# Performance work log

Hardware: AMD Instinct MI355X
Metric: run time of the kernel (lower is better)

## Reference

```python
import jax, jax.numpy as jnp
import numpy as np

B, N, D, NH, DFF = 16, 512, 1024, 16, 4096
DK = D // NH


def _layer_norm(x, eps=1e-5):
    mu = jnp.mean(x, axis=-1, keepdims=True)
    var = jnp.var(x, axis=-1, keepdims=True)
    return (x - mu) * jax.lax.rsqrt(var + eps)


def setup_inputs() -> dict:
    key = jax.random.key(0)
    ks = jax.random.split(key, 12)
    s = 0.02
    return {
        "H": jax.random.normal(ks[0], (B, N, D), jnp.float32),
        "shortest_path_matrix": jax.random.normal(ks[1], (B, N, N), jnp.float32),
        "Wq": s * jax.random.normal(ks[2], (NH, D, DK), jnp.float32),
        "bq": jnp.zeros((NH, DK), jnp.float32),
        "Wk": s * jax.random.normal(ks[3], (NH, D, DK), jnp.float32),
        "bk": jnp.zeros((NH, DK), jnp.float32),
        "Wv": s * jax.random.normal(ks[4], (NH, D, DK), jnp.float32),
        "bv": jnp.zeros((NH, DK), jnp.float32),
        "Wo": s * jax.random.normal(ks[5], (D, D), jnp.float32),
        "bo": jnp.zeros((D,), jnp.float32),
        "W1": s * jax.random.normal(ks[6], (D, DFF), jnp.float32),
        "b1": jnp.zeros((DFF,), jnp.float32),
        "W2": s * jax.random.normal(ks[7], (DFF, D), jnp.float32),
        "b2": jnp.zeros((D,), jnp.float32),
    }


def reference(H, shortest_path_matrix, Wq, bq, Wk, bk, Wv, bv, Wo, bo, W1, b1, W2, b2):
    ln1 = _layer_norm(H)  # [B,N,D]
    # per-head projections: [B,H,N,DK]
    Q = jnp.einsum('bnd,hdk->bhnk', ln1, Wq) + bq[None, :, None, :]
    K = jnp.einsum('bnd,hdk->bhnk', ln1, Wk) + bk[None, :, None, :]
    V = jnp.einsum('bnd,hdk->bhnk', ln1, Wv) + bv[None, :, None, :]
    scale = 1.0 / jnp.sqrt(jnp.asarray(DK, Q.dtype))
    scores = jnp.einsum('bhnk,bhmk->bhnm', Q, K) * scale + shortest_path_matrix[:, None, :, :]
    A = jax.nn.softmax(scores, axis=-1)
    O = jnp.einsum('bhnm,bhmk->bhnk', A, V)  # [B,H,N,DK]
    O = jnp.transpose(O, (0, 2, 1, 3)).reshape(O.shape[0], O.shape[2], -1)  # [B,N,D]
    attn_out = O @ Wo + bo
    x = attn_out + H
    h = jax.nn.relu(_layer_norm(x) @ W1 + b1)
    return x + h @ W2 + b2
```

## Files before the change

kernel.cpp:

```cpp
#include <hip/hip_runtime.h>

#define BB   16
#define NN   512
#define DD   1024
#define NHH  16
#define DKK  64
#define DFF  4096
#define MM   (BB*NN)

typedef _Float16 h16;
typedef h16  h16x8 __attribute__((ext_vector_type(8)));
typedef h16  h16x4 __attribute__((ext_vector_type(4)));
typedef float f32x4 __attribute__((ext_vector_type(4)));

#define AS1 __attribute__((address_space(1)))
#define AS3 __attribute__((address_space(3)))

__device__ __forceinline__ void gld16(h16* lds_dst, const h16* g_src) {
  __builtin_amdgcn_global_load_lds((const AS1 void*)g_src, (AS3 void*)lds_dst, 16, 0, 0);
}

__global__ __launch_bounds__(256) void ln_k(const float* __restrict__ in, h16* __restrict__ out)
{
  const int row = blockIdx.x;
  const int tid = threadIdx.x;
  const float4 v = ((const float4*)(in + (long)row * DD))[tid];
  float s  = v.x + v.y + v.z + v.w;
  float ss = v.x*v.x + v.y*v.y + v.z*v.z + v.w*v.w;
#pragma unroll
  for (int d = 32; d > 0; d >>= 1) { s += __shfl_down(s, d); ss += __shfl_down(ss, d); }
  __shared__ float red[8];
  const int wv = tid >> 6, ln = tid & 63;
  if (ln == 0) { red[wv] = s; red[4 + wv] = ss; }
  __syncthreads();
  s  = red[0] + red[1] + red[2] + red[3];
  ss = red[4] + red[5] + red[6] + red[7];
  const float mean = s * (1.0f / DD);
  const float var  = ss * (1.0f / DD) - mean * mean;
  const float rstd = rsqrtf(var + 1e-5f);
  h16x4 o;
  o[0] = (h16)((v.x - mean) * rstd);
  o[1] = (h16)((v.y - mean) * rstd);
  o[2] = (h16)((v.z - mean) * rstd);
  o[3] = (h16)((v.w - mean) * rstd);
  ((h16x4*)(out + (long)row * DD))[tid] = o;
}

__global__ __launch_bounds__(256) void tcast_k(const float* __restrict__ src, h16* __restrict__ dst,
                                               int R, int C, long sB, long dB)
{
  __shared__ float tile[32][33];
  const float* s = src + (long)blockIdx.z * sB;
  h16* d = dst + (long)blockIdx.z * dB;
  const int c0 = blockIdx.x * 32, r0 = blockIdx.y * 32;
  const int tx = threadIdx.x & 31, ty = threadIdx.x >> 5;
#pragma unroll
  for (int i = 0; i < 32; i += 8)
    tile[ty + i][tx] = s[(long)(r0 + ty + i) * C + c0 + tx];
  __syncthreads();
#pragma unroll
  for (int i = 0; i < 32; i += 8)
    d[(long)(c0 + ty + i) * R + r0 + tx] = (h16)tile[tx][ty + i];
}

template<int EPI>
__global__ __launch_bounds__(256) void gemm_k(
    const h16* __restrict__ A, const h16* __restrict__ Bt, int K, int Nc,
    const float* __restrict__ bias0, const float* __restrict__ bias1,
    h16* __restrict__ o0, h16* __restrict__ o1,
    float* __restrict__ of, const float* __restrict__ addsrc)
{
  __shared__ h16 Asb[3 * 4096];
  __shared__ h16 Bsb[3 * 4096];
  const int tid  = threadIdx.x;
  const int wave = tid >> 6, lane = tid & 63;
  const int lr = lane & 15, lq = lane >> 4;

  const int nxw = gridDim.x, nyw = gridDim.y;
  const int orig = blockIdx.x + nxw * blockIdx.y;
  const int xcd = orig & 7, sseq = orig >> 3;
  const int by = xcd * (nyw >> 3) + sseq / nxw;
  const int bx = sseq % nxw;
  const int m0 = by * 128, n0 = bx * 128;
  const int wr = (wave >> 1) * 64, wc = (wave & 1) * 64;

  const int c0 = tid,       r0 = c0 >> 2, s0 = ((c0 & 3) ^ ((c0 >> 3) & 3)) * 8;
  const int c1 = tid + 256, r1 = c1 >> 2, s1 = ((c1 & 3) ^ ((c1 >> 3) & 3)) * 8;

  int offA[4], offB[4];
#pragma unroll
  for (int i = 0; i < 4; ++i) {
    const int ra = wr + i * 16 + lr;
    const int rb = wc + i * 16 + lr;
    offA[i] = ra * 32 + (lq ^ ((ra >> 1) & 3)) * 8;
    offB[i] = rb * 32 + (lq ^ ((rb >> 1) & 3)) * 8;
  }

  f32x4 acc[4][4] = {};

  auto STAGE = [&](int k0, int bi) {
    h16* Ad = Asb + bi * 4096;
    h16* Bd = Bsb + bi * 4096;
    gld16(Ad + c0 * 8, A  + (long)(m0 + r0) * K + k0 + s0);
    gld16(Ad + c1 * 8, A  + (long)(m0 + r1) * K + k0 + s1);
    gld16(Bd + c0 * 8, Bt + (long)(n0 + r0) * K + k0 + s0);
    gld16(Bd + c1 * 8, Bt + (long)(n0 + r1) * K + k0 + s1);
  };

  const int nt = K >> 5;
  STAGE(0, 0);
  STAGE(32, 1);
  int cur = 0, nxt = 2;

  for (int t = 0; t < nt; ++t) {
    if (t + 2 < nt) {
      STAGE((t + 2) << 5, nxt);
      nxt = (nxt == 2) ? 0 : nxt + 1;
    }
    if (t + 2 < nt)      asm volatile("s_waitcnt vmcnt(8)" ::: "memory");
    else if (t + 1 < nt) asm volatile("s_waitcnt vmcnt(4)" ::: "memory");
    else                 asm volatile("s_waitcnt vmcnt(0)" ::: "memory");
    __builtin_amdgcn_sched_barrier(0);
    __builtin_amdgcn_s_barrier();
    asm volatile("" ::: "memory");

    const h16* Ac = Asb + cur * 4096;
    const h16* Bc = Bsb + cur * 4096;
    h16x8 af[4], bf[4];
#pragma unroll
    for (int i = 0; i < 4; ++i) {
      af[i] = *(const h16x8*)(Ac + offA[i]);
      bf[i] = *(const h16x8*)(Bc + offB[i]);
    }
    __builtin_amdgcn_s_setprio(1);
#pragma unroll
    for (int i = 0; i < 4; ++i)
#pragma unroll
      for (int j = 0; j < 4; ++j)
        acc[i][j] = __builtin_amdgcn_mfma_f32_16x16x32_f16(af[i], bf[j], acc[i][j], 0, 0, 0);
    __builtin_amdgcn_s_setprio(0);

    asm volatile("s_waitcnt lgkmcnt(0)" ::: "memory");
    __builtin_amdgcn_sched_barrier(0);
    __builtin_amdgcn_s_barrier();
    asm volatile("" ::: "memory");

    cur = (cur == 2) ? 0 : cur + 1;
  }

#pragma unroll
  for (int i = 0; i < 4; ++i) {
#pragma unroll
    for (int jn = 0; jn < 4; ++jn) {
#pragma unroll
      for (int j = 0; j < 4; ++j) {
        const int m   = m0 + wr + i * 16 + lq * 4 + j;
        const int col = n0 + wc + jn * 16 + lr;
        float v = acc[i][jn][j];
        if constexpr (EPI == 0) {
          const int w  = col >> 10;
          const int hh = (col >> 6) & 15, kk = col & 63;
          const int bidx = m >> 9, nq = m & 511;
          const int bcol = col & 1023;
          if (w == 0) o0[(((long)bidx * NHH + hh) * NN + nq) * DKK + kk] = (h16)(v + bias0[bcol]);
          else        o1[(((long)bidx * NHH + hh) * NN + nq) * DKK + kk] = (h16)(v + bias1[bcol]);
        } else if constexpr (EPI == 1) {
          of[(long)m * Nc + col] = v + bias0[col] + addsrc[(long)m * Nc + col];
        } else if constexpr (EPI == 2) {
          o0[(long)m * Nc + col] = (h16)fmaxf(v + bias0[col], 0.0f);
        } else if constexpr (EPI == 3) {
          of[(long)m * Nc + col] = v + bias0[col] + addsrc[(long)m * Nc + col];
        } else {
          const int bidx = col >> 9, nq = col & 511;
          o0[(((long)bidx * NHH + (m >> 6)) * DKK + (m & 63)) * NN + nq] = (h16)(v + bias0[m]);
        }
      }
    }
  }
}

__global__ __launch_bounds__(256) void attn_k(
    const h16* __restrict__ Qh, const h16* __restrict__ Kh, const h16* __restrict__ Vt,
    const float* __restrict__ spm, h16* __restrict__ Oh)
{
  __shared__ h16 Qs[128 * 64];
  __shared__ h16 Ks[64 * 64];
  __shared__ h16 Vts[64 * 64];
  __shared__ h16 Ps[4 * 32 * 64];
  const int tid  = threadIdx.x;
  const int wave = tid >> 6, lane = tid & 63;
  const int lr = lane & 15, lq = lane >> 4;
  const int b = blockIdx.z, h = blockIdx.y;
  const int q0 = blockIdx.x * 128;
  const long bh = (long)b * NHH + h;
  const h16* Qg = Qh + bh * NN * DKK;
  const h16* Kg = Kh + bh * NN * DKK;
  const h16* Vg = Vt + bh * DKK * NN;

#pragma unroll
  for (int r = 0; r < 4; ++r) {
    const int c = r * 256 + tid;
    gld16(Qs + c * 8, Qg + (long)(q0 + (c >> 3)) * DKK + (c & 7) * 8);
  }

  f32x4 acc[2][4] = {};
  float mrow[2][4], lsum[2][4];
#pragma unroll
  for (int a = 0; a < 2; ++a)
#pragma unroll
    for (int j = 0; j < 4; ++j) { mrow[a][j] = -3.0e38f; lsum[a][j] = 0.0f; }

  for (int kc = 0; kc < NN; kc += 64) {
#pragma unroll
    for (int r = 0; r < 2; ++r) {
      const int c = r * 256 + tid;
      const int row = c >> 3, sg = (c & 7) * 8;
      gld16(Ks  + c * 8, Kg + (long)(kc + row) * DKK + sg);
      gld16(Vts + c * 8, Vg + (long)row * NN + kc + sg);
    }
    __syncthreads();

    f32x4 s[2][4] = {};
#pragma unroll
    for (int ks = 0; ks < 2; ++ks) {
      h16x8 aq[2], bk4[4];
#pragma unroll
      for (int qm = 0; qm < 2; ++qm)
        aq[qm] = *(const h16x8*)(Qs + (wave * 32 + qm * 16 + lr) * 64 + ks * 32 + lq * 8);
#pragma unroll
      for (int kn = 0; kn < 4; ++kn)
        bk4[kn] = *(const h16x8*)(Ks + (kn * 16 + lr) * 64 + ks * 32 + lq * 8);
#pragma unroll
      for (int qm = 0; qm < 2; ++qm)
#pragma unroll
        for (int kn = 0; kn < 4; ++kn)
          s[qm][kn] = __builtin_amdgcn_mfma_f32_16x16x32_f16(aq[qm], bk4[kn], s[qm][kn], 0, 0, 0);
    }

    float pm[2][4];
#pragma unroll
    for (int qm = 0; qm < 2; ++qm)
#pragma unroll
      for (int j = 0; j < 4; ++j) pm[qm][j] = -3.0e38f;
#pragma unroll
    for (int qm = 0; qm < 2; ++qm)
#pragma unroll
      for (int kn = 0; kn < 4; ++kn)
#pragma unroll
        for (int j = 0; j < 4; ++j) {
          const int q = q0 + wave * 32 + qm * 16 + lq * 4 + j;
          const int key = kc + kn * 16 + lr;
          float v = s[qm][kn][j] * 0.125f + spm[((long)b * NN + q) * NN + key];
          s[qm][kn][j] = v;
          pm[qm][j] = fmaxf(pm[qm][j], v);
        }
#pragma unroll
    for (int qm = 0; qm < 2; ++qm)
#pragma unroll
      for (int j = 0; j < 4; ++j) {
#pragma unroll
        for (int d = 1; d < 16; d <<= 1) pm[qm][j] = fmaxf(pm[qm][j], __shfl_xor(pm[qm][j], d));
      }
    float corr[2][4];
#pragma unroll
    for (int qm = 0; qm < 2; ++qm)
#pragma unroll
      for (int j = 0; j < 4; ++j) {
        const float mn = fmaxf(mrow[qm][j], pm[qm][j]);
        corr[qm][j] = __expf(mrow[qm][j] - mn);
        mrow[qm][j] = mn;
        lsum[qm][j] *= corr[qm][j];
      }
    float rs[2][4] = {};
#pragma unroll
    for (int qm = 0; qm < 2; ++qm)
#pragma unroll
      for (int kn = 0; kn < 4; ++kn)
#pragma unroll
        for (int j = 0; j < 4; ++j) {
          const float pexp = __expf(s[qm][kn][j] - mrow[qm][j]);
          s[qm][kn][j] = pexp;
          rs[qm][j] += pexp;
        }
#pragma unroll
    for (int qm = 0; qm < 2; ++qm)
#pragma unroll
      for (int j = 0; j < 4; ++j) {
#pragma unroll
        for (int d = 1; d < 16; d <<= 1) rs[qm][j] += __shfl_xor(rs[qm][j], d);
        lsum[qm][j] += rs[qm][j];
      }
#pragma unroll
    for (int qm = 0; qm < 2; ++qm)
#pragma unroll
      for (int dn = 0; dn < 4; ++dn)
#pragma unroll
        for (int j = 0; j < 4; ++j) acc[qm][dn][j] *= corr[qm][j];

#pragma unroll
    for (int qm = 0; qm < 2; ++qm)
#pragma unroll
      for (int kn = 0; kn < 4; ++kn)
#pragma unroll
        for (int j = 0; j < 4; ++j)
          Ps[wave * 2048 + (qm * 16 + lq * 4 + j) * 64 + kn * 16 + lr] = (h16)s[qm][kn][j];

#pragma unroll
    for (int ks = 0; ks < 2; ++ks) {
      h16x8 ap[2], bv4[4];
#pragma unroll
      for (int qm = 0; qm < 2; ++qm)
        ap[qm] = *(const h16x8*)(Ps + wave * 2048 + (qm * 16 + lr) * 64 + ks * 32 + lq * 8);
#pragma unroll
      for (int dn = 0; dn < 4; ++dn)
        bv4[dn] = *(const h16x8*)(Vts + (dn * 16 + lr) * 64 + ks * 32 + lq * 8);
#pragma unroll
      for (int qm = 0; qm < 2; ++qm)
#pragma unroll
        for (int dn = 0; dn < 4; ++dn)
          acc[qm][dn] = __builtin_amdgcn_mfma_f32_16x16x32_f16(ap[qm], bv4[dn], acc[qm][dn], 0, 0, 0);
    }
    __syncthreads();
  }

  float rinv[2][4];
#pragma unroll
  for (int qm = 0; qm < 2; ++qm)
#pragma unroll
    for (int j = 0; j < 4; ++j) rinv[qm][j] = 1.0f / lsum[qm][j];
#pragma unroll
  for (int qm = 0; qm < 2; ++qm)
#pragma unroll
    for (int dn = 0; dn < 4; ++dn)
#pragma unroll
      for (int j = 0; j < 4; ++j) {
        const int q = q0 + wave * 32 + qm * 16 + lq * 4 + j;
        const int dk = dn * 16 + lr;
        Oh[((long)b * NN + q) * DD + h * DKK + dk] = (h16)(acc[qm][dn][j] * rinv[qm][j]);
      }
}

extern "C" void kernel_launch(void* const* d_in, const int* in_sizes, int n_in,
                              void* d_out, int out_size, void* d_ws, size_t ws_size,
                              hipStream_t stream)
{
  const float* H   = (const float*)d_in[0];
  const float* spm = (const float*)d_in[1];
  const float* Wq  = (const float*)d_in[2];
  const float* bq  = (const float*)d_in[3];
  const float* Wk  = (const float*)d_in[4];
  const float* bk  = (const float*)d_in[5];
  const float* Wv  = (const float*)d_in[6];
  const float* bv  = (const float*)d_in[7];
  const float* Wo  = (const float*)d_in[8];
  const float* bo  = (const float*)d_in[9];
  const float* W1  = (const float*)d_in[10];
  const float* b1  = (const float*)d_in[11];
  const float* W2  = (const float*)d_in[12];
  const float* b2  = (const float*)d_in[13];
  float* out = (float*)d_out;

  char* p = (char*)d_ws;
  auto alloc = [&](size_t bytes) { char* r = p; p += (bytes + 255) & ~(size_t)255; return r; };
  h16* ln1   = (h16*)alloc((size_t)MM * DD * 2);
  h16* wqkv  = (h16*)alloc((size_t)3 * DD * DD * 2);
  h16* wo_t  = (h16*)alloc((size_t)DD * DD * 2);
  h16* w1_t  = (h16*)alloc((size_t)DD * DFF * 2);
  h16* w2_t  = (h16*)alloc((size_t)DFF * DD * 2);
  h16* Qh    = (h16*)alloc((size_t)MM * DD * 2);
  h16* Kh    = (h16*)alloc((size_t)MM * DD * 2);
  h16* Vt    = (h16*)alloc((size_t)MM * DD * 2);
  h16* Oh    = (h16*)alloc((size_t)MM * DD * 2);
  float* x   = (float*)alloc((size_t)MM * DD * 4);
  h16* ln2 = ln1;
  h16* hff = Qh;

  ln_k<<<MM, 256, 0, stream>>>(H, ln1);
  tcast_k<<<dim3(2, 32, 16),  256, 0, stream>>>(Wq, wqkv,                 DD, DKK, (long)DD * DKK, (long)DKK * DD);
  tcast_k<<<dim3(2, 32, 16),  256, 0, stream>>>(Wk, wqkv + DD * DD,       DD, DKK, (long)DD * DKK, (long)DKK * DD);
  tcast_k<<<dim3(2, 32, 16),  256, 0, stream>>>(Wv, wqkv + 2 * DD * DD,   DD, DKK, (long)DD * DKK, (long)DKK * DD);
  tcast_k<<<dim3(32, 32, 1),  256, 0, stream>>>(Wo, wo_t, DD,  DD,  0, 0);
  tcast_k<<<dim3(128, 32, 1), 256, 0, stream>>>(W1, w1_t, DD,  DFF, 0, 0);
  tcast_k<<<dim3(32, 128, 1), 256, 0, stream>>>(W2, w2_t, DFF, DD,  0, 0);
  gemm_k<0><<<dim3(16, 64), 256, 0, stream>>>(ln1, wqkv, DD, 2 * DD, bq, bk, Qh, Kh, nullptr, nullptr);
  gemm_k<4><<<dim3(64, 8), 256, 0, stream>>>(wqkv + 2 * DD * DD, ln1, DD, MM, bv, nullptr, Vt, nullptr, nullptr, nullptr);
  attn_k<<<dim3(4, NHH, BB), 256, 0, stream>>>(Qh, Kh, Vt, spm, Oh);
  gemm_k<1><<<dim3(8, 64), 256, 0, stream>>>(Oh, wo_t, DD, DD, bo, nullptr, nullptr, nullptr, x, H);
  ln_k<<<MM, 256, 0, stream>>>(x, ln2);
  gemm_k<2><<<dim3(32, 64), 256, 0, stream>>>(ln2, w1_t, DD, DFF, b1, nullptr, hff, nullptr, nullptr, nullptr);
  gemm_k<3><<<dim3(8, 64), 256, 0, stream>>>(hff, w2_t, DFF, DD, b2, nullptr, nullptr, nullptr, out, x);
}
```

Before: 548.6 us.

## Double-buffer K/V tiles in attention with XOR-swizzled LDS and MFMA priority

The attention kernel now double-buffers the K and V^T tiles in shared memory, prefetching the next 64-key chunk while the current one is computed. Partial vmcnt waits and raw s_barrier replace the full __syncthreads. Q, K, V and P tiles use an XOR swizzle on 16-byte slots to cut LDS bank conflicts on the MFMA operand reads. s_setprio is raised around the MFMA blocks. This costs extra LDS, which may lower occupancy, and relies on a hand-tuned waitcnt count that must match the number of outstanding loads.

```diff
diff --git a/kernel.cpp b/kernel.cpp
--- a/kernel.cpp
+++ b/kernel.cpp
@@ -184,8 +184,8 @@
     const float* __restrict__ spm, h16* __restrict__ Oh)
 {
   __shared__ h16 Qs[128 * 64];
-  __shared__ h16 Ks[64 * 64];
-  __shared__ h16 Vts[64 * 64];
+  __shared__ h16 Ks[2][64 * 64];
+  __shared__ h16 Vts[2][64 * 64];
   __shared__ h16 Ps[4 * 32 * 64];
   const int tid  = threadIdx.x;
   const int wave = tid >> 6, lane = tid & 63;
@@ -200,8 +200,21 @@
 #pragma unroll
   for (int r = 0; r < 4; ++r) {
     const int c = r * 256 + tid;
-    gld16(Qs + c * 8, Qg + (long)(q0 + (c >> 3)) * DKK + (c & 7) * 8);
+    const int row = c >> 3, sl = c & 7;
+    gld16(Qs + c * 8, Qg + (long)(q0 + row) * DKK + ((sl ^ (row & 7)) * 8));
   }
+
+  auto STAGEKV = [&](int kc, int bi) {
+#pragma unroll
+    for (int r = 0; r < 2; ++r) {
+      const int c = r * 256 + tid;
+      const int row = c >> 3, sl = c & 7;
+      const int sg = (sl ^ (row & 7)) * 8;
+      gld16(&Ks[bi][c * 8],  Kg + (long)(kc + row) * DKK + sg);
+      gld16(&Vts[bi][c * 8], Vg + (long)row * NN + kc + sg);
+    }
+  };
+  STAGEKV(0, 0);
 
   f32x4 acc[2][4] = {};
   float mrow[2][4], lsum[2][4];
@@ -210,31 +223,43 @@
 #pragma unroll
     for (int j = 0; j < 4; ++j) { mrow[a][j] = -3.0e38f; lsum[a][j] = 0.0f; }
 
-  for (int kc = 0; kc < NN; kc += 64) {
-#pragma unroll
-    for (int r = 0; r < 2; ++r) {
-      const int c = r * 256 + tid;
-      const int row = c >> 3, sg = (c & 7) * 8;
-      gld16(Ks  + c * 8, Kg + (long)(kc + row) * DKK + sg);
-      gld16(Vts + c * 8, Vg + (long)row * NN + kc + sg);
-    }
-    __syncthreads();
+  const int NT = NN / 64;
+  for (int t = 0; t < NT; ++t) {
+    const int kc = t * 64;
+    if (t + 1 < NT) {
+      STAGEKV(kc + 64, (t + 1) & 1);
+      asm volatile("s_waitcnt vmcnt(4)" ::: "memory");
+    } else {
+      asm volatile("s_waitcnt vmcnt(0)" ::: "memory");
+    }
+    __builtin_amdgcn_sched_barrier(0);
+    __builtin_amdgcn_s_barrier();
+    asm volatile("" ::: "memory");
+
+    const h16* Kc = Ks[t & 1];
+    const h16* Vc = Vts[t & 1];
 
     f32x4 s[2][4] = {};
 #pragma unroll
     for (int ks = 0; ks < 2; ++ks) {
       h16x8 aq[2], bk4[4];
 #pragma unroll
-      for (int qm = 0; qm < 2; ++qm)
-        aq[qm] = *(const h16x8*)(Qs + (wave * 32 + qm * 16 + lr) * 64 + ks * 32 + lq * 8);
-#pragma unroll
-      for (int kn = 0; kn < 4; ++kn)
-        bk4[kn] = *(const h16x8*)(Ks + (kn * 16 + lr) * 64 + ks * 32 + lq * 8);
+      for (int qm = 0; qm < 2; ++qm) {
+        const int row = wave * 32 + qm * 16 + lr;
+        aq[qm] = *(const h16x8*)(Qs + row * 64 + ((ks * 4 + lq) ^ (row & 7)) * 8);
+      }
+#pragma unroll
+      for (int kn = 0; kn < 4; ++kn) {
+        const int row = kn * 16 + lr;
+        bk4[kn] = *(const h16x8*)(Kc + row * 64 + ((ks * 4 + lq) ^ (row & 7)) * 8);
+      }
+      __builtin_amdgcn_s_setprio(1);
 #pragma unroll
       for (int qm = 0; qm < 2; ++qm)
 #pragma unroll
         for (int kn = 0; kn < 4; ++kn)
           s[qm][kn] = __builtin_amdgcn_mfma_f32_16x16x32_f16(aq[qm], bk4[kn], s[qm][kn], 0, 0, 0);
+      __builtin_amdgcn_s_setprio(0);
     }
 
     float pm[2][4];
@@ -302,25 +327,38 @@
 #pragma unroll
       for (int kn = 0; kn < 4; ++kn)
 #pragma unroll
-        for (int j = 0; j < 4; ++j)
-          Ps[wave * 2048 + (qm * 16 + lq * 4 + j) * 64 + kn * 16 + lr] = (h16)s[qm][kn][j];
+        for (int j = 0; j < 4; ++j) {
+          const int row = qm * 16 + lq * 4 + j;
+          const int sl  = (kn * 2 + (lr >> 3)) ^ (row & 7);
+          Ps[wave * 2048 + row * 64 + sl * 8 + (lr & 7)] = (h16)s[qm][kn][j];
+        }
 
 #pragma unroll
     for (int ks = 0; ks < 2; ++ks) {
       h16x8 ap[2], bv4[4];
 #pragma unroll
-      for (int qm = 0; qm < 2; ++qm)
-        ap[qm] = *(const h16x8*)(Ps + wave * 2048 + (qm * 16 + lr) * 64 + ks * 32 + lq * 8);
-#pragma unroll
-      for (int dn = 0; dn < 4; ++dn)
-        bv4[dn] = *(const h16x8*)(Vts + (dn * 16 + lr) * 64 + ks * 32 + lq * 8);
+      for (int qm = 0; qm < 2; ++qm) {
+        const int row = qm * 16 + lr;
+        ap[qm] = *(const h16x8*)(Ps + wave * 2048 + row * 64 + ((ks * 4 + lq) ^ (row & 7)) * 8);
+      }
+#pragma unroll
+      for (int dn = 0; dn < 4; ++dn) {
+        const int row = dn * 16 + lr;
+        bv4[dn] = *(const h16x8*)(Vc + row * 64 + ((ks * 4 + lq) ^ (row & 7)) * 8);
+      }
+      __builtin_amdgcn_s_setprio(1);
 #pragma unroll
       for (int qm = 0; qm < 2; ++qm)
 #pragma unroll
         for (int dn = 0; dn < 4; ++dn)
           acc[qm][dn] = __builtin_amdgcn_mfma_f32_16x16x32_f16(ap[qm], bv4[dn], acc[qm][dn], 0, 0, 0);
-    }
-    __syncthreads();
+      __builtin_amdgcn_s_setprio(0);
+    }
+
+    asm volatile("s_waitcnt lgkmcnt(0)" ::: "memory");
+    __builtin_amdgcn_sched_barrier(0);
+    __builtin_amdgcn_s_barrier();
+    asm volatile("" ::: "memory");
   }
 
   float rinv[2][4];
```

After: 519.9 us. -5.2%, faster.
